# Optimization experiments

Measured on AMD Instinct MI355X. Metric: run time of the kernel, lower is better.

Reference implementation:

```python
import jax, jax.numpy as jnp
import numpy as np

B, T, D, H = 2, 2048, 1024, 16
DK = D // H


def setup_inputs() -> dict:
    key = jax.random.key(0)
    ks = jax.random.split(key, 9)
    s = 1.0 / np.sqrt(D)
    x = jax.random.normal(ks[0], (B, T, D), dtype=jnp.float32)
    # causal mask (1 = attend, 0 = masked), broadcast over batch and heads
    mask = jnp.tril(jnp.ones((T, T), dtype=jnp.int32))[None, None, :, :]
    Wq = jax.random.uniform(ks[1], (D, D), jnp.float32, -s, s)
    bq = jax.random.uniform(ks[2], (D,), jnp.float32, -s, s)
    Wk = jax.random.uniform(ks[3], (D, D), jnp.float32, -s, s)
    bk = jax.random.uniform(ks[4], (D,), jnp.float32, -s, s)
    Wv = jax.random.uniform(ks[5], (D, D), jnp.float32, -s, s)
    bv = jax.random.uniform(ks[6], (D,), jnp.float32, -s, s)
    Wo = jax.random.uniform(ks[7], (D, D), jnp.float32, -s, s)
    bo = jax.random.uniform(ks[8], (D,), jnp.float32, -s, s)
    return {"x": x, "mask": mask, "Wq": Wq, "bq": bq, "Wk": Wk, "bk": bk,
            "Wv": Wv, "bv": bv, "Wo": Wo, "bo": bo}


def reference(x, mask, Wq, bq, Wk, bk, Wv, bv, Wo, bo):
    # nn.Linear: y = x @ W.T + b
    q = (x @ Wq.T + bq).reshape(B, T, H, DK).transpose(0, 2, 1, 3)  # [B,H,T,DK]
    k = (x @ Wk.T + bk).reshape(B, T, H, DK).transpose(0, 2, 1, 3)
    v = (x @ Wv.T + bv).reshape(B, T, H, DK).transpose(0, 2, 1, 3)
    scores = jnp.einsum('bhqd,bhkd->bhqk', q, k) / np.sqrt(DK).astype(np.float32)
    scores = jnp.where(mask == 0, -jnp.inf, scores)
    attn = jax.nn.softmax(scores, axis=-1)
    out = jnp.einsum('bhqk,bhkd->bhqd', attn, v)  # [B,H,T,DK]
    out = out.transpose(0, 2, 1, 3).reshape(B, T, D)
    return out @ Wo.T + bo
```

## Files before the change

### kernel.cpp

```cpp
#include <hip/hip_runtime.h>

typedef unsigned short u16;
typedef unsigned int u32;
typedef unsigned long long u64;
typedef __attribute__((ext_vector_type(8))) short short8;
typedef __attribute__((ext_vector_type(4))) float f32x4;

#define B_ 2
#define T_ 2048
#define H_ 16
#define DK_ 64
#define QSCALE 0.18033688011112042f

__device__ __forceinline__ u16 f2bf(float f){
  unsigned u = __float_as_uint(f);
  return (u16)((u + 0x7fffu + ((u >> 16) & 1u)) >> 16);
}

__device__ __forceinline__ u32 cvtpk(float lo, float hi){
  u32 r;
  asm("v_cvt_pk_bf16_f32 %0, %1, %2" : "=v"(r) : "v"(lo), "v"(hi));
  return r;
}

#define EXP2(x) __expf(0.6931471805599453f * (x))

__device__ __forceinline__ short8 pack8(const f32x4 a, const f32x4 b){
  union { u32 u[4]; short8 s; } t;
  t.u[0] = cvtpk(a[0], a[1]); t.u[1] = cvtpk(a[2], a[3]);
  t.u[2] = cvtpk(b[0], b[1]); t.u[3] = cvtpk(b[2], b[3]);
  return t.s;
}

#if defined(__has_builtin)
#if __has_builtin(__builtin_amdgcn_global_load_lds)
#define HAS_GLLDS 1
#endif
#endif

#ifdef HAS_GLLDS
__device__ __forceinline__ void gl_lds16(const u16* g, u16* l){
  __builtin_amdgcn_global_load_lds(
      (__attribute__((address_space(1))) void*)(void*)g,
      (__attribute__((address_space(3))) void*)(void*)l, 16, 0, 0);
}
__device__ __forceinline__ void wait_vm4(){ asm volatile("s_waitcnt vmcnt(4)" ::: "memory"); }
__device__ __forceinline__ void wait_vm0(){ asm volatile("s_waitcnt vmcnt(0)" ::: "memory"); }
__device__ __forceinline__ void pipe_bar(){
  asm volatile("" ::: "memory");
  __builtin_amdgcn_s_barrier();
  asm volatile("" ::: "memory");
}
#else
__device__ __forceinline__ void wait_vm4(){}
__device__ __forceinline__ void wait_vm0(){}
__device__ __forceinline__ void pipe_bar(){ __syncthreads(); }
#endif

__global__ __launch_bounds__(256) void conv_all(
    const float* __restrict__ x, const float* __restrict__ wq, const float* __restrict__ wk,
    const float* __restrict__ wv, const float* __restrict__ wo,
    u16* __restrict__ xb, u16* __restrict__ wqb, u16* __restrict__ wkb,
    u16* __restrict__ wvb, u16* __restrict__ wob)
{
  int gid = blockIdx.x * 256 + threadIdx.x;
  const float* src; u16* dst; int off;
  if (gid < 1048576){ src = x; dst = xb; off = gid; }
  else {
    int t = gid - 1048576; int s = t >> 18; off = t & 262143;
    src = (s==0)?wq:((s==1)?wk:((s==2)?wv:wo));
    dst = (s==0)?wqb:((s==1)?wkb:((s==2)?wvb:wob));
  }
  float4 v = ((const float4*)src)[off];
  u64 r = (u64)f2bf(v.x) | ((u64)f2bf(v.y)<<16) | ((u64)f2bf(v.z)<<32) | ((u64)f2bf(v.w)<<48);
  ((u64*)dst)[off] = r;
}

__global__ __launch_bounds__(512, 2) void gemm_qkv8(
    const u16* __restrict__ A,
    const u16* __restrict__ W0, const u16* __restrict__ W1, const u16* __restrict__ W2,
    const float* __restrict__ b0, const float* __restrict__ b1, const float* __restrict__ b2,
    u16* __restrict__ o0, u16* __restrict__ o1, u16* __restrict__ o2)
{
  __shared__ u16 As[2][256 * 64];
  __shared__ u16 Bs[2][256 * 64];
  const int tid = threadIdx.x;
  const int w = tid >> 6, l = tid & 63;
  const int lr = l & 15, lg = l >> 4;
  const int sel = blockIdx.x >> 2;
  const int n0 = (blockIdx.x & 3) * 256, m0 = blockIdx.y * 256;
  const u16* Bw = (sel==0)?W0:((sel==1)?W1:W2);
  const float* bias = (sel==0)?b0:((sel==1)?b1:b2);
  u16* C = (sel==0)?o0:((sel==1)?o1:o2);
  const int wm = (w >> 2) * 128, wn = (w & 3) * 64;
  const int srow = l >> 3;
  const int schunk = ((l & 7) ^ (l >> 3)) * 8;
  const u16* Asrc = A  + (size_t)(m0 + srow) * 1024 + schunk;
  const u16* Bsrc = Bw + (size_t)(n0 + srow) * 1024 + schunk;

  auto SA = [&](int kt, int c, int pb){
    const int r0 = 32 * w + 8 * c;
#ifdef HAS_GLLDS
    gl_lds16(Asrc + (size_t)r0 * 1024 + kt * 64, &As[pb][r0 * 64]);
#else
    *(uint4*)&As[pb][r0 * 64 + l * 8] = *(const uint4*)(Asrc + (size_t)r0 * 1024 + kt * 64);
#endif
  };
  auto SB = [&](int kt, int c, int pb){
    const int r0 = 32 * w + 8 * c;
#ifdef HAS_GLLDS
    gl_lds16(Bsrc + (size_t)r0 * 1024 + kt * 64, &Bs[pb][r0 * 64]);
#else
    *(uint4*)&Bs[pb][r0 * 64 + l * 8] = *(const uint4*)(Bsrc + (size_t)r0 * 1024 + kt * 64);
#endif
  };

  f32x4 acc[8][4] = {};

#pragma unroll
  for (int c = 0; c < 4; ++c){ SA(0, c, 0); SB(0, c, 0); }
  wait_vm0();
  pipe_bar();

  for (int kt = 0; kt < 16; ++kt){
    const int pb = kt & 1;
    short8 bfa[4][2];
#pragma unroll
    for (int q = 0; q < 4; ++q){
      if (q == 0){
#pragma unroll
        for (int fn = 0; fn < 4; ++fn)
#pragma unroll
          for (int s = 0; s < 2; ++s)
            bfa[fn][s] = *(const short8*)&Bs[pb][(wn + 16*fn + lr) * 64 + (((4*s + lg) ^ (lr & 7)) << 3)];
      }
      short8 af[2][2];
#pragma unroll
      for (int mi = 0; mi < 2; ++mi)
#pragma unroll
        for (int s = 0; s < 2; ++s)
          af[mi][s] = *(const short8*)&As[pb][(wm + 16*(2*q + mi) + lr) * 64 + (((4*s + lg) ^ (lr & 7)) << 3)];
      if (kt < 15){ SA(kt + 1, q, pb ^ 1); SB(kt + 1, q, pb ^ 1); }
      __builtin_amdgcn_s_barrier();
      __builtin_amdgcn_s_setprio(1);
#pragma unroll
      for (int mi = 0; mi < 2; ++mi)
#pragma unroll
        for (int fn = 0; fn < 4; ++fn)
#pragma unroll
          for (int s = 0; s < 2; ++s)
            acc[2*q + mi][fn] = __builtin_amdgcn_mfma_f32_16x16x32_bf16(
                af[mi][s], bfa[fn][s], acc[2*q + mi][fn], 0, 0, 0);
      __builtin_amdgcn_s_setprio(0);
      if (q == 3 && kt < 15) wait_vm0();
      __builtin_amdgcn_s_barrier();
    }
  }

  float bv[4];
#pragma unroll
  for (int fn = 0; fn < 4; ++fn) bv[fn] = bias[n0 + wn + 16*fn + lr];
#pragma unroll
  for (int fm = 0; fm < 8; ++fm)
#pragma unroll
    for (int r = 0; r < 4; ++r){
      const int trow = m0 + wm + 16*fm + 4*lg + r;
#pragma unroll
      for (int fn = 0; fn < 4; ++fn){
        float v = acc[fm][fn][r] + bv[fn];
        int n = n0 + wn + 16*fn + lr;
        if (sel == 0){
          C[(size_t)trow * 1024 + n] = f2bf(v * QSCALE);
        } else if (sel == 1){
          int nsw = (n & ~63) | ((n & 63) ^ ((trow & 7) << 3));
          C[(size_t)trow * 1024 + nsw] = f2bf(v);
        } else {
          C[(size_t)trow * 1024 + n] = f2bf(v);
        }
      }
    }
}

__global__ __launch_bounds__(256, 3) void gemm_o(
    const u16* __restrict__ A, const u16* __restrict__ Bw,
    const float* __restrict__ bias, float* __restrict__ C)
{
  __shared__ u16 As[3 * 4096];
  __shared__ u16 Bs[3 * 4096];
  const int tid = threadIdx.x;
  const int n0 = blockIdx.x * 128, m0 = blockIdx.y * 128;
  const int w = tid>>6, l = tid&63;
  const int lr = l&15, lg = l>>4;
  const int wm = (w&1)*64, wn = (w>>1)*64;
  const int scol = ((l & 3) ^ ((l >> 3) & 3)) * 8;
  const u16* Ab = A  + (size_t)m0*1024 + (size_t)(l>>2)*1024 + scol;
  const u16* Bb = Bw + (size_t)n0*1024 + (size_t)(l>>2)*1024 + scol;
  const int rsw = (lr >> 1) & 3;
  f32x4 acc[4][4] = {};

  auto STAGE = [&](int t, int pb){
#pragma unroll
    for (int i = 0; i < 2; ++i){
      int c = w*2 + i;
#ifdef HAS_GLLDS
      gl_lds16(Ab + (size_t)(16*c)*1024 + t*32, &As[pb*4096 + c*512]);
      gl_lds16(Bb + (size_t)(16*c)*1024 + t*32, &Bs[pb*4096 + c*512]);
#else
      *(uint4*)&As[pb*4096 + c*512 + l*8] = *(const uint4*)(Ab + (size_t)(16*c)*1024 + t*32);
      *(uint4*)&Bs[pb*4096 + c*512 + l*8] = *(const uint4*)(Bb + (size_t)(16*c)*1024 + t*32);
#endif
    }
  };

  STAGE(0, 0); STAGE(1, 1);
  wait_vm4();
  pipe_bar();
  for (int it = 0; it < 32; ++it){
    const int pb = it % 3;
    if (it < 30) STAGE(it + 2, (it + 2) % 3);
    short8 af[4], bf[4];
#pragma unroll
    for (int mi=0;mi<4;++mi) af[mi] = *(const short8*)&As[pb*4096 + (wm+16*mi+lr)*32 + 8*(lg ^ rsw)];
#pragma unroll
    for (int ni=0;ni<4;++ni) bf[ni] = *(const short8*)&Bs[pb*4096 + (wn+16*ni+lr)*32 + 8*(lg ^ rsw)];
#pragma unroll
    for (int mi=0;mi<4;++mi)
#pragma unroll
      for (int ni=0;ni<4;++ni)
        acc[mi][ni] = __builtin_amdgcn_mfma_f32_16x16x32_bf16(af[mi], bf[ni], acc[mi][ni], 0,0,0);
    if (it < 31){
      if (it < 30) wait_vm4();
      else         wait_vm0();
      pipe_bar();
    }
  }

  float bv[4];
#pragma unroll
  for (int ni=0;ni<4;++ni) bv[ni] = bias[n0+wn+16*ni+lr];
#pragma unroll
  for (int mi=0;mi<4;++mi)
#pragma unroll
    for (int r=0;r<4;++r){
      const int trow = m0 + wm + 16*mi + 4*lg + r;
#pragma unroll
      for (int ni=0;ni<4;++ni)
        C[(size_t)trow*1024 + n0 + wn + 16*ni + lr] = acc[mi][ni][r] + bv[ni];
    }
}

__global__ __launch_bounds__(256) void transpose_v128(const u16* __restrict__ V,
                                                      u16* __restrict__ VT){
  __shared__ u16 L[128 * 72];
  const int tid = threadIdx.x;
  const int tc = blockIdx.x, h = blockIdx.y, b = blockIdx.z;
#pragma unroll
  for (int p = 0; p < 4; ++p){
    int row = (tid >> 3) + 32 * p, g = tid & 7;
    *(uint4*)&L[row * 72 + g * 8] =
        *(const uint4*)(V + ((size_t)(b * T_ + tc * 128 + row) * H_ + h) * DK_ + g * 8);
  }
  __syncthreads();
#pragma unroll
  for (int p = 0; p < 4; ++p){
    int d = tid >> 2, g8 = (tid & 3) + 4 * p;
    union { uint4 u; u16 s[8]; } tv;
#pragma unroll
    for (int i = 0; i < 8; ++i){
      int pp = 8 * g8 + i;
      int tl = 32 * (pp >> 5) + 16 * ((pp >> 2) & 1) + 4 * ((pp >> 3) & 3) + (pp & 3);
      tv.s[i] = L[tl * 72 + d];
    }
    *(uint4*)(VT + ((size_t)(b * H_ + h) * DK_ + d) * T_ + tc * 128 + ((8 * g8) ^ ((d & 7) << 3))) = tv.u;
  }
}

__global__ __launch_bounds__(256, 2) void attn_v7(
    const u16* __restrict__ Q, const u16* __restrict__ K,
    const u16* __restrict__ VT, u16* __restrict__ O)
{
  __shared__ u16 Ks[2][128 * 64];
  __shared__ u16 VTs[2][64 * 128];
  const int tid = threadIdx.x;
  const int w = tid >> 6, l = tid & 63;
  const int lr = l & 15, lg = l >> 4;
  const int h = blockIdx.y, b = blockIdx.z;
  const int qtb = (b == 0) ? blockIdx.x : (15 - blockIdx.x);
  const int q0 = qtb * 128;
  const int wrow0 = q0 + 32 * w;
  const size_t kbase = ((size_t)(b * T_) * H_ + h) * DK_;
  const size_t vbase = (size_t)(b * H_ + h) * DK_ * (size_t)T_;

  auto STAGE = [&](int kt, int pb){
#pragma unroll
    for (int p = 0; p < 4; ++p){
      int kr0 = 32 * w + 8 * p;
#ifdef HAS_GLLDS
      gl_lds16(K + kbase + (size_t)(kt * 128 + kr0 + (l >> 3)) * 1024 + (l & 7) * 8,
               &Ks[pb][kr0 * 64]);
#else
      *(uint4*)&Ks[pb][(kr0 + (l >> 3)) * 64 + (l & 7) * 8] =
          *(const uint4*)(K + kbase + (size_t)(kt * 128 + kr0 + (l >> 3)) * 1024 + (l & 7) * 8);
#endif
    }
#pragma unroll
    for (int p = 0; p < 4; ++p){
      int dr0 = 16 * w + 4 * p;
#ifdef HAS_GLLDS
      gl_lds16(VT + vbase + (size_t)(dr0 + (l >> 4)) * T_ + kt * 128 + (l & 15) * 8,
               &VTs[pb][dr0 * 128]);
#else
      *(uint4*)&VTs[pb][(dr0 + (l >> 4)) * 128 + (l & 15) * 8] =
          *(const uint4*)(VT + vbase + (size_t)(dr0 + (l >> 4)) * T_ + kt * 128 + (l & 15) * 8);
#endif
    }
  };

  short8 qf[2][2];
#pragma unroll
  for (int mi = 0; mi < 2; ++mi)
#pragma unroll
    for (int s = 0; s < 2; ++s)
      qf[mi][s] = *(const short8*)(Q + kbase + (size_t)(wrow0 + 16 * mi + lr) * 1024 + s * 32 + 8 * lg);

  f32x4 acc[2][4] = {};
  float lsum[2] = {0.f, 0.f};
  const int ktend = qtb;

  STAGE(0, 0);
  __syncthreads();
  for (int kt = 0; kt <= ktend; ++kt){
    const int pb = kt & 1;
    if (kt < ktend) STAGE(kt + 1, pb ^ 1);
    const bool diag = (kt == ktend);
    short8 pf[2][4];
#pragma unroll
    for (int jh = 0; jh < 2; ++jh){
      short8 kf[4][2];
#pragma unroll
      for (int j = 0; j < 4; ++j)
#pragma unroll
        for (int s = 0; s < 2; ++s)
          kf[j][s] = *(const short8*)&Ks[pb][((4 * jh + j) * 16 + lr) * 64 + (((4 * s + lg) ^ (lr & 7)) << 3)];
#pragma unroll
      for (int mi = 0; mi < 2; ++mi){
        f32x4 pr[4];
        float lacc = 0.f;
        const int lim = 32 * w + 16 * mi + lr;
#pragma unroll
        for (int j = 0; j < 4; ++j){
          const int j0 = 4 * jh + j;
          f32x4 z = {};
          z = __builtin_amdgcn_mfma_f32_16x16x32_bf16(kf[j][0], qf[mi][0], z, 0, 0, 0);
          z = __builtin_amdgcn_mfma_f32_16x16x32_bf16(kf[j][1], qf[mi][1], z, 0, 0, 0);
#pragma unroll
          for (int r = 0; r < 4; ++r){
            float e = EXP2(z[r]);
            if (diag && (16 * j0 + 4 * lg + r > lim)) e = 0.f;
            pr[j][r] = e;
            lacc += e;
          }
        }
        lsum[mi] += lacc;
        pf[mi][2 * jh]     = pack8(pr[0], pr[1]);
        pf[mi][2 * jh + 1] = pack8(pr[2], pr[3]);
      }
    }
#pragma unroll
    for (int ks = 0; ks < 4; ++ks)
#pragma unroll
      for (int d0 = 0; d0 < 4; ++d0){
        short8 vf = *(const short8*)&VTs[pb][(d0 * 16 + lr) * 128 + (((4 * ks + lg) ^ (lr & 7)) << 3)];
        acc[0][d0] = __builtin_amdgcn_mfma_f32_16x16x32_bf16(pf[0][ks], vf, acc[0][d0], 0, 0, 0);
        acc[1][d0] = __builtin_amdgcn_mfma_f32_16x16x32_bf16(pf[1][ks], vf, acc[1][d0], 0, 0, 0);
      }
    __syncthreads();
  }

#pragma unroll
  for (int mi = 0; mi < 2; ++mi){
    float v = lsum[mi];
    v += __shfl_xor(v, 16);
    v += __shfl_xor(v, 32);
    float inv = 1.0f / v;
    float invr[4];
#pragma unroll
    for (int r = 0; r < 4; ++r) invr[r] = __shfl(inv, 4 * lg + r);
#pragma unroll
    for (int d0 = 0; d0 < 4; ++d0)
#pragma unroll
      for (int r = 0; r < 4; ++r){
        float ov = acc[mi][d0][r] * invr[r];
        O[kbase + (size_t)(wrow0 + 16 * mi + 4 * lg + r) * 1024 + d0 * 16 + lr] = f2bf(ov);
      }
  }
}

extern "C" void kernel_launch(void* const* d_in, const int* in_sizes, int n_in,
                              void* d_out, int out_size, void* d_ws, size_t ws_size,
                              hipStream_t stream)
{
  const float* x  = (const float*)d_in[0];
  const float* Wq = (const float*)d_in[2];
  const float* bq = (const float*)d_in[3];
  const float* Wk = (const float*)d_in[4];
  const float* bk = (const float*)d_in[5];
  const float* Wv = (const float*)d_in[6];
  const float* bv = (const float*)d_in[7];
  const float* Wo = (const float*)d_in[8];
  const float* bo = (const float*)d_in[9];

  char* ws = (char*)d_ws;
  u16* xb  = (u16*)(ws + 0);
  u16* wqb = (u16*)(ws + 8388608);
  u16* wkb = (u16*)(ws + 10485760);
  u16* wvb = (u16*)(ws + 12582912);
  u16* wob = (u16*)(ws + 14680064);
  u16* qb  = (u16*)(ws + 16777216);
  u16* kb  = (u16*)(ws + 25165824);
  u16* vb  = (u16*)(ws + 33554432);
  u16* vtb = xb;
  u16* ab  = vb;

  conv_all<<<8192, 256, 0, stream>>>(x, Wq, Wk, Wv, Wo, xb, wqb, wkb, wvb, wob);

  gemm_qkv8<<<dim3(12, 16), 512, 0, stream>>>(
      xb, wqb, wkb, wvb, bq, bk, bv, qb, kb, vb);

  transpose_v128<<<dim3(T_/128, H_, B_), 256, 0, stream>>>(vb, vtb);

  attn_v7<<<dim3(T_/128, H_, B_), 256, 0, stream>>>(qb, kb, vtb, ab);

  gemm_o<<<dim3(8, 32), 256, 0, stream>>>(ab, wob, bo, (float*)d_out);
}
```

Measured before the change: 117.7 us.

## Prefetch two K-tiles ahead in QKV GEMM with fewer barriers

After: 119.2 us. About the same (+1.3%).

```diff
diff --git a/kernel.cpp b/kernel.cpp
--- a/kernel.cpp
+++ b/kernel.cpp
@@ -44,6 +44,7 @@
       (__attribute__((address_space(1))) void*)(void*)g,
       (__attribute__((address_space(3))) void*)(void*)l, 16, 0, 0);
 }
+__device__ __forceinline__ void wait_vm8(){ asm volatile("s_waitcnt vmcnt(8)" ::: "memory"); }
 __device__ __forceinline__ void wait_vm4(){ asm volatile("s_waitcnt vmcnt(4)" ::: "memory"); }
 __device__ __forceinline__ void wait_vm0(){ asm volatile("s_waitcnt vmcnt(0)" ::: "memory"); }
 __device__ __forceinline__ void pipe_bar(){
@@ -52,6 +53,7 @@
   asm volatile("" ::: "memory");
 }
 #else
+__device__ __forceinline__ void wait_vm8(){}
 __device__ __forceinline__ void wait_vm4(){}
 __device__ __forceinline__ void wait_vm0(){}
 __device__ __forceinline__ void pipe_bar(){ __syncthreads(); }
@@ -93,55 +95,48 @@
   const float* bias = (sel==0)?b0:((sel==1)?b1:b2);
   u16* C = (sel==0)?o0:((sel==1)?o1:o2);
   const int wm = (w >> 2) * 128, wn = (w & 3) * 64;
-  const int srow = l >> 3;
-  const int schunk = ((l & 7) ^ (l >> 3)) * 8;
-  const u16* Asrc = A  + (size_t)(m0 + srow) * 1024 + schunk;
-  const u16* Bsrc = Bw + (size_t)(n0 + srow) * 1024 + schunk;
-
-  auto SA = [&](int kt, int c, int pb){
-    const int r0 = 32 * w + 8 * c;
+  const int schunk = ((l & 7) ^ ((l >> 3) & 7)) * 8;
+  const u16* Asrc = A  + (size_t)(m0 + (l >> 3)) * 1024 + schunk;
+  const u16* Bsrc = Bw + (size_t)(n0 + (l >> 3)) * 1024 + schunk;
+  const int rsw = lr & 7;
+
+  auto STAGE = [&](int kt, int pb){
+#pragma unroll
+    for (int i = 0; i < 4; ++i){
+      const int r0 = 64 * i + 8 * w;
 #ifdef HAS_GLLDS
-    gl_lds16(Asrc + (size_t)r0 * 1024 + kt * 64, &As[pb][r0 * 64]);
+      gl_lds16(Asrc + (size_t)r0 * 1024 + kt * 64, &As[pb][r0 * 64]);
+      gl_lds16(Bsrc + (size_t)r0 * 1024 + kt * 64, &Bs[pb][r0 * 64]);
 #else
-    *(uint4*)&As[pb][r0 * 64 + l * 8] = *(const uint4*)(Asrc + (size_t)r0 * 1024 + kt * 64);
-#endif
+      *(uint4*)&As[pb][r0 * 64 + l * 8] = *(const uint4*)(Asrc + (size_t)r0 * 1024 + kt * 64);
+      *(uint4*)&Bs[pb][r0 * 64 + l * 8] = *(const uint4*)(Bsrc + (size_t)r0 * 1024 + kt * 64);
+#endif
+    }
   };
-  auto SB = [&](int kt, int c, int pb){
-    const int r0 = 32 * w + 8 * c;
-#ifdef HAS_GLLDS
-    gl_lds16(Bsrc + (size_t)r0 * 1024 + kt * 64, &Bs[pb][r0 * 64]);
-#else
-    *(uint4*)&Bs[pb][r0 * 64 + l * 8] = *(const uint4*)(Bsrc + (size_t)r0 * 1024 + kt * 64);
-#endif
-  };
 
   f32x4 acc[8][4] = {};
 
-#pragma unroll
-  for (int c = 0; c < 4; ++c){ SA(0, c, 0); SB(0, c, 0); }
-  wait_vm0();
+  STAGE(0, 0);
+  STAGE(1, 1);
+  wait_vm8();
   pipe_bar();
 
   for (int kt = 0; kt < 16; ++kt){
     const int pb = kt & 1;
     short8 bfa[4][2];
 #pragma unroll
+    for (int fn = 0; fn < 4; ++fn)
+#pragma unroll
+      for (int s = 0; s < 2; ++s)
+        bfa[fn][s] = *(const short8*)&Bs[pb][(wn + 16*fn + lr) * 64 + (((4*s + lg) ^ rsw) << 3)];
+#pragma unroll
     for (int q = 0; q < 4; ++q){
-      if (q == 0){
-#pragma unroll
-        for (int fn = 0; fn < 4; ++fn)
-#pragma unroll
-          for (int s = 0; s < 2; ++s)
-            bfa[fn][s] = *(const short8*)&Bs[pb][(wn + 16*fn + lr) * 64 + (((4*s + lg) ^ (lr & 7)) << 3)];
-      }
       short8 af[2][2];
 #pragma unroll
       for (int mi = 0; mi < 2; ++mi)
 #pragma unroll
         for (int s = 0; s < 2; ++s)
-          af[mi][s] = *(const short8*)&As[pb][(wm + 16*(2*q + mi) + lr) * 64 + (((4*s + lg) ^ (lr & 7)) << 3)];
-      if (kt < 15){ SA(kt + 1, q, pb ^ 1); SB(kt + 1, q, pb ^ 1); }
-      __builtin_amdgcn_s_barrier();
+          af[mi][s] = *(const short8*)&As[pb][(wm + 16*(2*q + mi) + lr) * 64 + (((4*s + lg) ^ rsw) << 3)];
       __builtin_amdgcn_s_setprio(1);
 #pragma unroll
       for (int mi = 0; mi < 2; ++mi)
@@ -152,8 +147,16 @@
             acc[2*q + mi][fn] = __builtin_amdgcn_mfma_f32_16x16x32_bf16(
                 af[mi][s], bfa[fn][s], acc[2*q + mi][fn], 0, 0, 0);
       __builtin_amdgcn_s_setprio(0);
-      if (q == 3 && kt < 15) wait_vm0();
-      __builtin_amdgcn_s_barrier();
+    }
+    if (kt < 15){
+      pipe_bar();
+      if (kt < 14){
+        STAGE(kt + 2, pb);
+        wait_vm8();
+      } else {
+        wait_vm0();
+      }
+      pipe_bar();
     }
   }
 
```
